# Kernel optimization log

Hardware: AMD Instinct MI355X
Metric: run time of the kernel (lower is better)

Reference implementation:

```python
import jax, jax.numpy as jnp
import numpy as np

N_NODES = 100000
N_EDGES = 3200000
F_IN = 128
HIDDEN = 64
C = 7


def sage_conv(x, src, dst, W_l, W_r, b, n_nodes):
    # PyG SAGEConv (mean aggr, root_weight=True):
    # out = lin_l(mean_{j in N(i)} x_j) + lin_r(x_i)
    msg = x[src]  # [E, F] gather of source-node features
    s = jax.ops.segment_sum(msg, dst, num_segments=n_nodes)  # [N, F]
    cnt = jax.ops.segment_sum(jnp.ones((src.shape[0], 1), x.dtype), dst,
                              num_segments=n_nodes)  # [N, 1]
    aggr = s / jnp.maximum(cnt, 1.0)  # degree-0 nodes -> 0, like PyG scatter-mean
    return aggr @ W_l.T + x @ W_r.T + b


def setup_inputs() -> dict:
    key = jax.random.key(0)
    ks = jax.random.split(key, 8)
    x = jax.random.normal(ks[0], (N_NODES, F_IN), dtype=jnp.float32)
    edge_index = jax.random.randint(ks[1], (2, N_EDGES), 0, N_NODES, dtype=jnp.int64)
    # Glorot-ish scaled params
    W1_l = jax.random.normal(ks[2], (HIDDEN, F_IN), dtype=jnp.float32) / np.sqrt(F_IN)
    W1_r = jax.random.normal(ks[3], (HIDDEN, F_IN), dtype=jnp.float32) / np.sqrt(F_IN)
    b1 = jnp.zeros((HIDDEN,), dtype=jnp.float32)
    W2_l = jax.random.normal(ks[4], (C, HIDDEN), dtype=jnp.float32) / np.sqrt(HIDDEN)
    W2_r = jax.random.normal(ks[5], (C, HIDDEN), dtype=jnp.float32) / np.sqrt(HIDDEN)
    b2 = jnp.zeros((C,), dtype=jnp.float32)
    return {"x": x, "edge_index": edge_index,
            "W1_l": W1_l, "W1_r": W1_r, "b1": b1,
            "W2_l": W2_l, "W2_r": W2_r, "b2": b2}


def reference(x, edge_index, W1_l, W1_r, b1, W2_l, W2_r, b2):
    src, dst = edge_index[0], edge_index[1]
    h = sage_conv(x, src, dst, W1_l, W1_r, b1, N_NODES)
    h = jax.nn.relu(h)
    # dropout(p=0.5, training=False) -> identity (eval mode)
    h = sage_conv(h, src, dst, W2_l, W2_r, b2, N_NODES)
    return jax.nn.log_softmax(h, axis=1)
```

## Files before the change

kernel.cpp:

```cpp
#include <hip/hip_runtime.h>
#include <math.h>

#define NN 100000
#define NE 3200000
#define FIN 128
#define HID 64
#define NC 7
#define BW 512
#define NBUC 196
#define CAP 20480
#define CHUNK 8192
#define NCHUNK ((NE + CHUNK - 1) / CHUNK)
#define PROJB ((NN + 127) / 128)

typedef __attribute__((ext_vector_type(8))) short bhalf8;
typedef __attribute__((ext_vector_type(4))) float f32x4;

__device__ __forceinline__ unsigned int f2bf(float x) {
    unsigned int u = __float_as_uint(x);
    return (u + 0x7fffu + ((u >> 16) & 1u)) >> 16;
}
__device__ __forceinline__ float bf_lo(unsigned int u) {
    return __uint_as_float(u << 16);
}
__device__ __forceinline__ float bf_hi(unsigned int u) {
    return __uint_as_float(u & 0xffff0000u);
}
__device__ __forceinline__ int swz(int row, int win) {
    return (win & 8) | ((win ^ row) & 7);
}

__global__ __launch_bounds__(256) void k_init(int* __restrict__ gcur,
                                              const float* __restrict__ W1l,
                                              const float* __restrict__ W1r,
                                              unsigned short* __restrict__ wb) {
    int b = blockIdx.x, t = threadIdx.x;
    if (b == 0) {
        if (t < NBUC) gcur[t] = t * CAP;
    } else {
#pragma unroll
        for (int e = 0; e < 4; ++e) {
            int idx = (b - 1) * 1024 + e * 256 + t;
            float v = (idx < 8192) ? W1l[idx] : W1r[idx - 8192];
            wb[idx] = (unsigned short)f2bf(v);
        }
    }
}

union SmemU {
    unsigned short xls[128 * 128];
    struct {
        unsigned int pay[CHUNK];
        int h[NBUC];
        int lcur[NBUC];
        unsigned char buc[CHUNK];
    } a;
};

__global__ __launch_bounds__(256) void k_pa_proj(const int* __restrict__ src,
                                                 const int* __restrict__ dst,
                                                 int* __restrict__ gcur,
                                                 unsigned int* __restrict__ ebuf,
                                                 const float* __restrict__ x,
                                                 const unsigned short* __restrict__ wb,
                                                 unsigned int* __restrict__ p1b,
                                                 float* __restrict__ r1) {
    __shared__ SmemU smem;
    int t = threadIdx.x;
    if (blockIdx.x < NCHUNK) {
        for (int i = t; i < NBUC; i += 256) smem.a.h[i] = 0;
        __syncthreads();
        int base = blockIdx.x * CHUNK;
        int cnt = min(CHUNK, NE - base);
        for (int i = t; i < cnt; i += 256) {
            int s = src[base + i];
            int d = dst[base + i];
            int b = d >> 9;
            smem.a.pay[i] = ((unsigned)(d & 511) << 17) | (unsigned)s;
            smem.a.buc[i] = (unsigned char)b;
            atomicAdd(&smem.a.h[b], 1);
        }
        __syncthreads();
        for (int i = t; i < NBUC; i += 256)
            smem.a.lcur[i] = smem.a.h[i] ? atomicAdd(&gcur[i], smem.a.h[i]) : 0;
        __syncthreads();
        for (int i = t; i < cnt; i += 256) {
            int p = atomicAdd(&smem.a.lcur[smem.a.buc[i]], 1);
            ebuf[p] = smem.a.pay[i];
        }
    } else {
        int n0 = (blockIdx.x - NCHUNK) * 128;
#pragma unroll
        for (int u = 0; u < 8; ++u) {
            int fid = u * 256 + t;
            int row = fid >> 4;
            int win = fid & 15;
            int n = n0 + row;
            uint4 w = make_uint4(0u, 0u, 0u, 0u);
            if (n < NN) {
                const float4* xp = (const float4*)&x[(size_t)n * 128 + win * 8];
                float4 v0 = xp[0], v1 = xp[1];
                w.x = f2bf(v0.x) | (f2bf(v0.y) << 16);
                w.y = f2bf(v0.z) | (f2bf(v0.w) << 16);
                w.z = f2bf(v1.x) | (f2bf(v1.y) << 16);
                w.w = f2bf(v1.z) | (f2bf(v1.w) << 16);
            }
            *(uint4*)((char*)smem.xls + row * 256 + swz(row, win) * 16) = w;
        }
        __syncthreads();
        int wv = t >> 6;
        int l = t & 63;
        int lr = l & 15;
        int lg = l >> 4;
        f32x4 acc[2][8];
#pragma unroll
        for (int rt = 0; rt < 2; ++rt)
#pragma unroll
            for (int ct = 0; ct < 8; ++ct) acc[rt][ct] = (f32x4)0.f;
        bhalf8 afr[2], bfr[8];
        for (int ks = 0; ks < 4; ++ks) {
#pragma unroll
            for (int rt = 0; rt < 2; ++rt) {
                int row = (wv * 2 + rt) * 16 + lr;
                int win = ks * 4 + lg;
                afr[rt] = *(bhalf8*)((char*)smem.xls + row * 256 + swz(row, win) * 16);
            }
#pragma unroll
            for (int ct = 0; ct < 8; ++ct)
                bfr[ct] = *(const bhalf8*)&wb[(ct * 16 + lr) * 128 + ks * 32 + lg * 8];
#pragma unroll
            for (int ct = 0; ct < 8; ++ct) {
                acc[0][ct] = __builtin_amdgcn_mfma_f32_16x16x32_bf16(
                    afr[0], bfr[ct], acc[0][ct], 0, 0, 0);
                acc[1][ct] = __builtin_amdgcn_mfma_f32_16x16x32_bf16(
                    afr[1], bfr[ct], acc[1][ct], 0, 0, 0);
            }
        }
        unsigned short* p1h = (unsigned short*)p1b;
#pragma unroll
        for (int rt = 0; rt < 2; ++rt) {
#pragma unroll
            for (int j = 0; j < 4; ++j) {
                int n = n0 + (wv * 2 + rt) * 16 + lg * 4 + j;
                if (n < NN) {
#pragma unroll
                    for (int ct = 0; ct < 8; ++ct) {
                        float vv = acc[rt][ct][j];
                        int ch = ct * 16 + lr;
                        if (ct < 4)
                            p1h[(size_t)n * 64 + ch] = (unsigned short)f2bf(vv);
                        else
                            r1[(size_t)n * 64 + (ch - 64)] = vv;
                    }
                }
            }
        }
    }
}

__global__ __launch_bounds__(512) void k_passB(const unsigned int* __restrict__ ebuf,
                                               const int* __restrict__ gcur,
                                               int* __restrict__ offs,
                                               int* __restrict__ cnti,
                                               int* __restrict__ skey) {
    __shared__ int lcnt[BW];
    __shared__ int lcur[BW];
    __shared__ int s2[256];
    int b = blockIdx.x, t = threadIdx.x;
    int beg = b * CAP, end = gcur[b];
    lcnt[t] = 0;
    __syncthreads();
    for (int i = beg + t; i < end; i += 512)
        atomicAdd(&lcnt[ebuf[i] >> 17], 1);
    __syncthreads();
    int c0 = 0, c1 = 0;
    if (t < 256) {
        c0 = lcnt[2 * t];
        c1 = lcnt[2 * t + 1];
        s2[t] = c0 + c1;
    }
    __syncthreads();
    for (int d = 1; d < 256; d <<= 1) {
        int a = 0;
        if (t < 256 && t >= d) a = s2[t - d];
        __syncthreads();
        if (t < 256) s2[t] += a;
        __syncthreads();
    }
    if (t < 256) {
        int excl = s2[t] - (c0 + c1);
        int o0 = beg + excl;
        int o1 = o0 + c0;
        lcur[2 * t] = o0;
        lcur[2 * t + 1] = o1;
        int n0 = b * BW + 2 * t;
        if (n0 < NN)     { offs[n0] = o0;     cnti[n0] = c0; }
        if (n0 + 1 < NN) { offs[n0 + 1] = o1; cnti[n0 + 1] = c1; }
    }
    __syncthreads();
    for (int i = beg + t; i < end; i += 512) {
        unsigned v = ebuf[i];
        int p = atomicAdd(&lcur[v >> 17], 1);
        skey[p] = (int)(v & 0x1FFFFu);
    }
}

__global__ __launch_bounds__(256) void k_agg1(const unsigned int* __restrict__ p1b,
                                              float* __restrict__ r1,
                                              const int* __restrict__ skey,
                                              const int* __restrict__ offs,
                                              const int* __restrict__ cnti,
                                              const float* __restrict__ b1) {
    int n = (blockIdx.x * 256 + threadIdx.x) >> 6;
    int l = threadIdx.x & 63;
    if (n >= NN) return;
    int half = l >> 5;
    int i32 = l & 31;
    int off = offs[n];
    int dc = cnti[n];
    float a0 = 0.f, a1 = 0.f;
    int e = half;
    for (; e + 14 < dc; e += 16) {
        int s0 = skey[off + e];
        int s1 = skey[off + e + 2];
        int s2 = skey[off + e + 4];
        int s3 = skey[off + e + 6];
        int s4 = skey[off + e + 8];
        int s5 = skey[off + e + 10];
        int s6 = skey[off + e + 12];
        int s7 = skey[off + e + 14];
        unsigned v0 = p1b[(size_t)s0 * 32 + i32];
        unsigned v1 = p1b[(size_t)s1 * 32 + i32];
        unsigned v2 = p1b[(size_t)s2 * 32 + i32];
        unsigned v3 = p1b[(size_t)s3 * 32 + i32];
        unsigned v4 = p1b[(size_t)s4 * 32 + i32];
        unsigned v5 = p1b[(size_t)s5 * 32 + i32];
        unsigned v6 = p1b[(size_t)s6 * 32 + i32];
        unsigned v7 = p1b[(size_t)s7 * 32 + i32];
        a0 += bf_lo(v0); a1 += bf_hi(v0);
        a0 += bf_lo(v1); a1 += bf_hi(v1);
        a0 += bf_lo(v2); a1 += bf_hi(v2);
        a0 += bf_lo(v3); a1 += bf_hi(v3);
        a0 += bf_lo(v4); a1 += bf_hi(v4);
        a0 += bf_lo(v5); a1 += bf_hi(v5);
        a0 += bf_lo(v6); a1 += bf_hi(v6);
        a0 += bf_lo(v7); a1 += bf_hi(v7);
    }
    for (; e + 6 < dc; e += 8) {
        int s0 = skey[off + e];
        int s1 = skey[off + e + 2];
        int s2 = skey[off + e + 4];
        int s3 = skey[off + e + 6];
        unsigned v0 = p1b[(size_t)s0 * 32 + i32];
        unsigned v1 = p1b[(size_t)s1 * 32 + i32];
        unsigned v2 = p1b[(size_t)s2 * 32 + i32];
        unsigned v3 = p1b[(size_t)s3 * 32 + i32];
        a0 += bf_lo(v0); a1 += bf_hi(v0);
        a0 += bf_lo(v1); a1 += bf_hi(v1);
        a0 += bf_lo(v2); a1 += bf_hi(v2);
        a0 += bf_lo(v3); a1 += bf_hi(v3);
    }
    for (; e < dc; e += 2) {
        int s0 = skey[off + e];
        unsigned v0 = p1b[(size_t)s0 * 32 + i32];
        a0 += bf_lo(v0); a1 += bf_hi(v0);
    }
    a0 += __shfl_xor(a0, 32);
    a1 += __shfl_xor(a1, 32);
    float ca = __shfl(a0, l >> 1);
    float cb = __shfl(a1, l >> 1);
    float acc = (l & 1) ? cb : ca;

    float inv = (dc > 0) ? 1.f / (float)dc : 0.f;
    float h = fmaxf(acc * inv + r1[(size_t)n * 64 + l] + b1[l], 0.f);
    r1[(size_t)n * 64 + l] = h;
}

__global__ __launch_bounds__(256) void k_proj2(const float* __restrict__ h,
                                               const float* __restrict__ W2l,
                                               const float* __restrict__ W2r,
                                               float* __restrict__ p2,
                                               float* __restrict__ r2) {
    __shared__ float swl[NC][64];
    __shared__ float swr[NC][64];
    int t = threadIdx.x;
    for (int i = t; i < NC * 64; i += 256) {
        swl[i >> 6][i & 63] = W2l[i];
        swr[i >> 6][i & 63] = W2r[i];
    }
    __syncthreads();
    int n = blockIdx.x * 256 + t;
    if (n >= NN) return;
    float al[NC], ar[NC];
#pragma unroll
    for (int c = 0; c < NC; ++c) { al[c] = 0.f; ar[c] = 0.f; }
    const float4* H = (const float4*)(h + (size_t)n * 64);
#pragma unroll
    for (int q = 0; q < 16; ++q) {
        float4 u = H[q];
        int k = q * 4;
#pragma unroll
        for (int c = 0; c < NC; ++c) {
            al[c] += u.x * swl[c][k] + u.y * swl[c][k + 1] +
                     u.z * swl[c][k + 2] + u.w * swl[c][k + 3];
            ar[c] += u.x * swr[c][k] + u.y * swr[c][k + 1] +
                     u.z * swr[c][k + 2] + u.w * swr[c][k + 3];
        }
    }
#pragma unroll
    for (int c = 0; c < NC; ++c) {
        p2[(size_t)n * 8 + c] = al[c];
        r2[(size_t)n * NC + c] = ar[c];
    }
}

__global__ __launch_bounds__(256) void k_agg2f(const float* __restrict__ p2,
                                               const float* __restrict__ r2,
                                               const int* __restrict__ skey,
                                               const int* __restrict__ offs,
                                               const int* __restrict__ cnti,
                                               const float* __restrict__ b2,
                                               float* __restrict__ out) {
    int tid = blockIdx.x * 256 + threadIdx.x;
    int n = tid >> 3;
    int c = tid & 7;
    if (n >= NN) return;
    bool act = (c < NC);
    int off = offs[n];
    int dc = cnti[n];
    int i = off, end = off + dc;
    float acc = 0.f;
    for (; i + 7 < end; i += 8) {
        int s0 = skey[i],     s1 = skey[i + 1], s2 = skey[i + 2], s3 = skey[i + 3];
        int s4 = skey[i + 4], s5 = skey[i + 5], s6 = skey[i + 6], s7 = skey[i + 7];
        if (act) {
            float x0 = p2[(size_t)s0 * 8 + c];
            float x1 = p2[(size_t)s1 * 8 + c];
            float x2 = p2[(size_t)s2 * 8 + c];
            float x3 = p2[(size_t)s3 * 8 + c];
            float x4 = p2[(size_t)s4 * 8 + c];
            float x5 = p2[(size_t)s5 * 8 + c];
            float x6 = p2[(size_t)s6 * 8 + c];
            float x7 = p2[(size_t)s7 * 8 + c];
            acc += x0 + x1 + x2 + x3 + x4 + x5 + x6 + x7;
        }
    }
    for (; i + 3 < end; i += 4) {
        int s0 = skey[i], s1 = skey[i + 1], s2 = skey[i + 2], s3 = skey[i + 3];
        if (act) {
            acc += p2[(size_t)s0 * 8 + c];
            acc += p2[(size_t)s1 * 8 + c];
            acc += p2[(size_t)s2 * 8 + c];
            acc += p2[(size_t)s3 * 8 + c];
        }
    }
    for (; i < end; ++i) if (act) acc += p2[(size_t)skey[i] * 8 + c];
    float inv = (dc > 0) ? 1.f / (float)dc : 0.f;
    float v = act ? (acc * inv + r2[(size_t)n * NC + c] + b2[c]) : -INFINITY;
    float m = v;
#pragma unroll
    for (int d = 1; d < 8; d <<= 1) m = fmaxf(m, __shfl_xor(m, d));
    float ev = act ? expf(v - m) : 0.f;
    float s = ev;
#pragma unroll
    for (int d = 1; d < 8; d <<= 1) s += __shfl_xor(s, d);
    if (act) out[(size_t)n * NC + c] = v - m - logf(s);
}

extern "C" void kernel_launch(void* const* d_in, const int* in_sizes, int n_in,
                              void* d_out, int out_size, void* d_ws, size_t ws_size,
                              hipStream_t stream) {
    const float* x   = (const float*)d_in[0];
    const int*   ei  = (const int*)d_in[1];
    const float* W1l = (const float*)d_in[2];
    const float* W1r = (const float*)d_in[3];
    const float* b1  = (const float*)d_in[4];
    const float* W2l = (const float*)d_in[5];
    const float* W2r = (const float*)d_in[6];
    const float* b2  = (const float*)d_in[7];
    float* out = (float*)d_out;

    const int* src = ei;
    const int* dst = ei + NE;

    int* gcur  = (int*)d_ws;
    int* cnti  = gcur + 256;
    int* offs  = cnti + NN;
    unsigned int* ebuf = (unsigned int*)(offs + NN);
    int* skey  = (int*)(ebuf + (size_t)NBUC * CAP);
    unsigned short* wb = (unsigned short*)(skey + (size_t)NBUC * CAP);
    unsigned int* p1b = (unsigned int*)((int*)wb + 8192);
    float* r1  = (float*)(p1b + (size_t)NN * 32);
    float* p2  = r1 + (size_t)NN * HID;
    float* r2  = p2 + (size_t)NN * 8;

    k_init   <<<17, 256, 0, stream>>>(gcur, W1l, W1r, wb);
    k_pa_proj<<<NCHUNK + PROJB, 256, 0, stream>>>(src, dst, gcur, ebuf,
                                                  x, wb, p1b, r1);
    k_passB  <<<NBUC, 512, 0, stream>>>(ebuf, gcur, offs, cnti, skey);
    k_agg1   <<<(NN * 64 + 255) / 256, 256, 0, stream>>>(p1b, r1, skey, offs,
                                                         cnti, b1);
    k_proj2  <<<(NN + 255) / 256, 256, 0, stream>>>(r1, W2l, W2r, p2, r2);
    k_agg2f  <<<(NN * 8 + 255) / 256, 256, 0, stream>>>(p2, r2, skey, offs,
                                                        cnti, b2, out);
}
```

Before: 181.2 us.

## Split layer-1 aggregation across eight feature groups per node

```diff
diff --git a/kernel.cpp b/kernel.cpp
--- a/kernel.cpp
+++ b/kernel.cpp
@@ -205,75 +205,50 @@
     }
 }
 
-__global__ __launch_bounds__(256) void k_agg1(const unsigned int* __restrict__ p1b,
-                                              float* __restrict__ r1,
-                                              const int* __restrict__ skey,
-                                              const int* __restrict__ offs,
-                                              const int* __restrict__ cnti,
-                                              const float* __restrict__ b1) {
-    int n = (blockIdx.x * 256 + threadIdx.x) >> 6;
+__global__ __launch_bounds__(256) void k_agg1g(const unsigned int* __restrict__ p1b,
+                                               float* __restrict__ r1,
+                                               const int* __restrict__ skey,
+                                               const int* __restrict__ offs,
+                                               const int* __restrict__ cnti,
+                                               const float* __restrict__ b1) {
+    int gidx = blockIdx.x;
+    int g = gidx & 7;
+    int n = (gidx >> 3) * 4 + (threadIdx.x >> 6);
     int l = threadIdx.x & 63;
     if (n >= NN) return;
-    int half = l >> 5;
-    int i32 = l & 31;
+    int e16 = l >> 2;
+    int q = (l & 3) + g * 4;
     int off = offs[n];
     int dc = cnti[n];
     float a0 = 0.f, a1 = 0.f;
-    int e = half;
-    for (; e + 14 < dc; e += 16) {
+    int e = e16;
+    for (; e + 16 < dc; e += 32) {
         int s0 = skey[off + e];
-        int s1 = skey[off + e + 2];
-        int s2 = skey[off + e + 4];
-        int s3 = skey[off + e + 6];
-        int s4 = skey[off + e + 8];
-        int s5 = skey[off + e + 10];
-        int s6 = skey[off + e + 12];
-        int s7 = skey[off + e + 14];
-        unsigned v0 = p1b[(size_t)s0 * 32 + i32];
-        unsigned v1 = p1b[(size_t)s1 * 32 + i32];
-        unsigned v2 = p1b[(size_t)s2 * 32 + i32];
-        unsigned v3 = p1b[(size_t)s3 * 32 + i32];
-        unsigned v4 = p1b[(size_t)s4 * 32 + i32];
-        unsigned v5 = p1b[(size_t)s5 * 32 + i32];
-        unsigned v6 = p1b[(size_t)s6 * 32 + i32];
-        unsigned v7 = p1b[(size_t)s7 * 32 + i32];
+        int s1 = skey[off + e + 16];
+        unsigned v0 = p1b[(size_t)s0 * 32 + q];
+        unsigned v1 = p1b[(size_t)s1 * 32 + q];
         a0 += bf_lo(v0); a1 += bf_hi(v0);
         a0 += bf_lo(v1); a1 += bf_hi(v1);
-        a0 += bf_lo(v2); a1 += bf_hi(v2);
-        a0 += bf_lo(v3); a1 += bf_hi(v3);
-        a0 += bf_lo(v4); a1 += bf_hi(v4);
-        a0 += bf_lo(v5); a1 += bf_hi(v5);
-        a0 += bf_lo(v6); a1 += bf_hi(v6);
-        a0 += bf_lo(v7); a1 += bf_hi(v7);
-    }
-    for (; e + 6 < dc; e += 8) {
+    }
+    for (; e < dc; e += 16) {
         int s0 = skey[off + e];
-        int s1 = skey[off + e + 2];
-        int s2 = skey[off + e + 4];
-        int s3 = skey[off + e + 6];
-        unsigned v0 = p1b[(size_t)s0 * 32 + i32];
-        unsigned v1 = p1b[(size_t)s1 * 32 + i32];
-        unsigned v2 = p1b[(size_t)s2 * 32 + i32];
-        unsigned v3 = p1b[(size_t)s3 * 32 + i32];
+        unsigned v0 = p1b[(size_t)s0 * 32 + q];
         a0 += bf_lo(v0); a1 += bf_hi(v0);
-        a0 += bf_lo(v1); a1 += bf_hi(v1);
-        a0 += bf_lo(v2); a1 += bf_hi(v2);
-        a0 += bf_lo(v3); a1 += bf_hi(v3);
-    }
-    for (; e < dc; e += 2) {
-        int s0 = skey[off + e];
-        unsigned v0 = p1b[(size_t)s0 * 32 + i32];
-        a0 += bf_lo(v0); a1 += bf_hi(v0);
-    }
-    a0 += __shfl_xor(a0, 32);
-    a1 += __shfl_xor(a1, 32);
-    float ca = __shfl(a0, l >> 1);
-    float cb = __shfl(a1, l >> 1);
-    float acc = (l & 1) ? cb : ca;
-
-    float inv = (dc > 0) ? 1.f / (float)dc : 0.f;
-    float h = fmaxf(acc * inv + r1[(size_t)n * 64 + l] + b1[l], 0.f);
-    r1[(size_t)n * 64 + l] = h;
+    }
+#pragma unroll
+    for (int d = 4; d < 64; d <<= 1) {
+        a0 += __shfl_xor(a0, d);
+        a1 += __shfl_xor(a1, d);
+    }
+    float va = __shfl(a0, l >> 1);
+    float vb = __shfl(a1, l >> 1);
+    if (l < 8) {
+        int ch = g * 8 + l;
+        float acc = (l & 1) ? vb : va;
+        float inv = (dc > 0) ? 1.f / (float)dc : 0.f;
+        float h = fmaxf(acc * inv + r1[(size_t)n * 64 + ch] + b1[ch], 0.f);
+        r1[(size_t)n * 64 + ch] = h;
+    }
 }
 
 __global__ __launch_bounds__(256) void k_proj2(const float* __restrict__ h,
@@ -398,8 +373,8 @@
     k_pa_proj<<<NCHUNK + PROJB, 256, 0, stream>>>(src, dst, gcur, ebuf,
                                                   x, wb, p1b, r1);
     k_passB  <<<NBUC, 512, 0, stream>>>(ebuf, gcur, offs, cnti, skey);
-    k_agg1   <<<(NN * 64 + 255) / 256, 256, 0, stream>>>(p1b, r1, skey, offs,
-                                                         cnti, b1);
+    k_agg1g  <<<8 * ((NN + 3) / 4), 256, 0, stream>>>(p1b, r1, skey, offs,
+                                                      cnti, b1);
     k_proj2  <<<(NN + 255) / 256, 256, 0, stream>>>(r1, W2l, W2r, p2, r2);
     k_agg2f  <<<(NN * 8 + 255) / 256, 256, 0, stream>>>(p2, r2, skey, offs,
                                                         cnti, b2, out);
```

Measured after the change: 472.3 us. 2.61x slower.
